# Kernel optimization log

Measured on AMD Instinct MI355X. Metric: run time of the kernel, lower is better.

Reference implementation:

```python
import jax, jax.numpy as jnp
import numpy as np
import math

B, T, D = 2, 2048, 1024
H, NL, DF = 16, 6, 4096
HD = D // H
EPS = 1e-5

def layer_norm(x, w, b):
    mu = jnp.mean(x, axis=-1, keepdims=True)
    var = jnp.mean((x - mu) ** 2, axis=-1, keepdims=True)
    return (x - mu) * jax.lax.rsqrt(var + EPS) * w + b

def setup_inputs() -> dict:
    key = jax.random.key(0)
    ks = jax.random.split(key, 12)
    def w(k, shape, scale=0.02):
        return jax.random.normal(k, shape, dtype=jnp.float32) * scale
    inp = {
        'sequences': jax.random.normal(ks[0], (B, T, D), dtype=jnp.float32),
        'Wq': w(ks[1], (NL, D, D)), 'bq': jnp.zeros((NL, D), jnp.float32),
        'Wk': w(ks[2], (NL, D, D)), 'bk': jnp.zeros((NL, D), jnp.float32),
        'Wv': w(ks[3], (NL, D, D)), 'bv': jnp.zeros((NL, D), jnp.float32),
        'Wo': w(ks[4], (NL, D, D)), 'bo': jnp.zeros((NL, D), jnp.float32),
        'Wz': w(ks[5], (NL, D, D)), 'bz': jnp.zeros((NL, D), jnp.float32),
        'Wr': w(ks[6], (NL, D, D)), 'br': jnp.zeros((NL, D), jnp.float32),
        'W1': w(ks[7], (NL, D, DF)), 'b1': jnp.zeros((NL, DF), jnp.float32),
        'W2': w(ks[8], (NL, DF, D)), 'b2': jnp.zeros((NL, D), jnp.float32),
        'ln1_w': jnp.ones((NL, D), jnp.float32), 'ln1_b': jnp.zeros((NL, D), jnp.float32),
        'ln2_w': jnp.ones((NL, D), jnp.float32), 'ln2_b': jnp.zeros((NL, D), jnp.float32),
        'lnf_w': jnp.ones((D,), jnp.float32), 'lnf_b': jnp.zeros((D,), jnp.float32),
    }
    return inp

def reference(sequences, Wq, bq, Wk, bk, Wv, bv, Wo, bo, Wz, bz, Wr, br,
              W1, b1, W2, b2, ln1_w, ln1_b, ln2_w, ln2_b, lnf_w, lnf_b):
    scale = 1.0 / math.sqrt(HD)
    causal = jnp.tril(jnp.ones((T, T), dtype=bool))  # mask[L:L+T, :L+T] with L=0
    x = sequences
    src = x
    for i in range(NL):
        xn = layer_norm(x, ln1_w[i], ln1_b[i])
        # QKV -> [B, H, T, HD]
        q = (xn @ Wq[i] + bq[i]).reshape(B, T, H, HD).transpose(0, 2, 1, 3)
        k = (xn @ Wk[i] + bk[i]).reshape(B, T, H, HD).transpose(0, 2, 1, 3)
        v = (xn @ Wv[i] + bv[i]).reshape(B, T, H, HD).transpose(0, 2, 1, 3)
        att = jnp.einsum('bhqd,bhkd->bhqk', q, k) * scale
        att = jnp.where(causal, att, -jnp.inf)
        att = jax.nn.softmax(att, axis=-1)
        y = jnp.einsum('bhqk,bhkd->bhqd', att, v)
        y = y.transpose(0, 2, 1, 3).reshape(B, T, D)
        x_attn = y @ Wo[i] + bo[i]
        z = jax.nn.sigmoid(xn @ Wz[i] + bz[i])
        r = jax.nn.sigmoid(xn @ Wr[i] + br[i])
        h_tilde = jnp.tanh(r * x_attn)
        x = (1.0 - z) * x + z * h_tilde
        xm = layer_norm(x, ln2_w[i], ln2_b[i])
        mlp = jax.nn.gelu(xm @ W1[i] + b1[i], approximate=False) @ W2[i] + b2[i]
        x = (1.0 - z) * x + z * mlp
        x = x + src
    x = layer_norm(x, lnf_w, lnf_b)
    return x
```

## Files before the change

### kernel.cpp

```cpp
#include <hip/hip_runtime.h>
#include <hip/hip_bf16.h>
#include <math.h>

#define B_ 2
#define T_ 2048
#define D_ 1024
#define H_ 16
#define NL_ 6
#define DF_ 4096
#define HD_ 64
#define M_ (B_*T_)

typedef __bf16 bf16;
typedef __attribute__((ext_vector_type(8))) __bf16 bf16x8;
typedef __attribute__((ext_vector_type(4))) float f32x4;
typedef __attribute__((ext_vector_type(16))) float f32x16;
typedef __attribute__((ext_vector_type(4))) unsigned u32x4;

#define BAR() __builtin_amdgcn_s_barrier()
#define LGKM0() asm volatile("s_waitcnt lgkmcnt(0)" ::: "memory")
#define VMC(n) asm volatile("s_waitcnt vmcnt(" #n ")" ::: "memory")

__device__ __forceinline__ void gload_lds16(const void* g, void* l) {
    __builtin_amdgcn_global_load_lds((const __attribute__((address_space(1))) void*)g,
                                     (__attribute__((address_space(3))) void*)l, 16, 0, 0);
}

__device__ __forceinline__ unsigned pk2(float a, float b) {
    bf16 lo = (bf16)a, hb = (bf16)b;
    return (unsigned)__builtin_bit_cast(unsigned short, lo) |
           ((unsigned)__builtin_bit_cast(unsigned short, hb) << 16);
}

__device__ __forceinline__ float4 ld4bf(const bf16* p) {
    float4 o;
    o.x = (float)p[0]; o.y = (float)p[1]; o.z = (float)p[2]; o.w = (float)p[3];
    return o;
}

template<bool OUT_BF16>
__global__ __launch_bounds__(256) void ln_kernel(const float* __restrict__ x,
        const float* __restrict__ w, const float* __restrict__ b,
        void* __restrict__ out) {
    const int row = blockIdx.x;
    const int t = threadIdx.x;
    const float4 xv = *(const float4*)(x + (long)row * D_ + t * 4);
    float s  = xv.x + xv.y + xv.z + xv.w;
    float sq = xv.x*xv.x + xv.y*xv.y + xv.z*xv.z + xv.w*xv.w;
    #pragma unroll
    for (int m = 32; m; m >>= 1) { s += __shfl_xor(s, m); sq += __shfl_xor(sq, m); }
    __shared__ float red[8];
    const int wid = t >> 6, lid = t & 63;
    if (lid == 0) { red[wid] = s; red[wid + 4] = sq; }
    __syncthreads();
    s  = red[0] + red[1] + red[2] + red[3];
    sq = red[4] + red[5] + red[6] + red[7];
    const float mu   = s * (1.0f / D_);
    const float var  = sq * (1.0f / D_) - mu * mu;
    const float rstd = rsqrtf(var + 1e-5f);
    const float4 wv = *(const float4*)(w + t * 4);
    const float4 bv = *(const float4*)(b + t * 4);
    float o0 = (xv.x - mu) * rstd * wv.x + bv.x;
    float o1 = (xv.y - mu) * rstd * wv.y + bv.y;
    float o2 = (xv.z - mu) * rstd * wv.z + bv.z;
    float o3 = (xv.w - mu) * rstd * wv.w + bv.w;
    if (OUT_BF16) {
        bf16* o = (bf16*)out + (long)row * D_ + t * 4;
        o[0] = (bf16)o0; o[1] = (bf16)o1; o[2] = (bf16)o2; o[3] = (bf16)o3;
    } else {
        float* o = (float*)out + (long)row * D_ + t * 4;
        o[0] = o0; o[1] = o1; o[2] = o2; o[3] = o3;
    }
}

__global__ __launch_bounds__(256) void wconv_all(
        const float* __restrict__ Wq, const float* __restrict__ Wk,
        const float* __restrict__ Wv, const float* __restrict__ Wz,
        const float* __restrict__ Wr, const float* __restrict__ Wo,
        const float* __restrict__ W1, const float* __restrict__ W2,
        bf16* __restrict__ wt) {
    __shared__ float s[32][33];
    const int bid = blockIdx.x;
    const float* src; bf16* dst; int t, K, nlg;
    if (bid < 6144) {
        const int m = bid >> 10; t = bid & 1023; K = 1024; nlg = 5;
        switch (m) {
            case 0: src = Wq; dst = wt; break;
            case 1: src = Wk; dst = wt + (1u << 20); break;
            case 2: src = Wv; dst = wt + (2u << 20); break;
            case 3: src = Wz; dst = wt + (3u << 20); break;
            case 4: src = Wr; dst = wt + (4u << 20); break;
            default: src = Wo; dst = wt + (5u << 20); break;
        }
    } else if (bid < 10240) {
        t = bid - 6144; K = 1024; nlg = 7; src = W1; dst = wt + (6u << 20);
    } else {
        t = bid - 10240; K = 4096; nlg = 5; src = W2; dst = wt + (10u << 20);
    }
    const int N = 1 << (nlg + 5);
    const int k0 = (t >> nlg) * 32, n0 = (t & ((1 << nlg) - 1)) * 32;
    const int c = threadIdx.x & 31, r8 = threadIdx.x >> 5;
    #pragma unroll
    for (int it = 0; it < 4; it++)
        s[r8 + it*8][c] = src[(long)(k0 + r8 + it*8) * N + n0 + c];
    __syncthreads();
    #pragma unroll
    for (int it = 0; it < 4; it++)
        dst[(long)(n0 + r8 + it*8) * K + k0 + c] = (bf16)s[c][r8 + it*8];
}

#define MFMA16(a, b, c) __builtin_amdgcn_mfma_f32_16x16x32_bf16(a, b, c, 0, 0, 0)
#define MFMA32(a, b, c) __builtin_amdgcn_mfma_f32_32x32x16_bf16(a, b, c, 0, 0, 0)

__device__ __forceinline__ void gemm128_core(const bf16* __restrict__ A, const bf16* __restrict__ Bt,
        const int Ks, const int NT, const int m0, const int n0, char* lds, f32x4 (&acc)[4][4]) {
    const int tid = threadIdx.x;
    const int lane = tid & 63, w = tid >> 6;
    const int wm = w >> 1, wn = w & 1;
    const int cl = lane & 15, gl = lane >> 4;
    const int srow = lane >> 2;
    const int sxc = (((lane & 3) ^ ((lane >> 3) & 3)) << 3);
    const bf16* pa0 = A  + (size_t)(m0 + w * 32 + srow) * Ks + sxc;
    const bf16* pa1 = pa0 + (size_t)16 * Ks;
    const bf16* pb  = Bt + (size_t)(n0 + w * 16 + srow) * Ks + sxc;
    char* laA = lds + w * 2048;
    char* laB = lds + 32768 + w * 1024;

#define STG(KT, BUF) do { \
    gload_lds16(pa0 + (size_t)(KT) * 32, laA + (BUF) * 16384); \
    gload_lds16(pa1 + (size_t)(KT) * 32, laA + (BUF) * 16384 + 1024); \
    gload_lds16(pb  + (size_t)(KT) * 32, laB + (BUF) * 8192); } while (0)

    STG(0, 0); STG(1, 1);
    VMC(3);

    const int xo  = ((gl ^ ((cl >> 1) & 3)) << 4);
    const int rdA = (wm * 64 + cl) * 64 + xo;
    const int rdB = (wn * 64 + cl) * 64 + xo;

    for (int kt = 0; kt < NT; ++kt) {
        const int buf = kt & 1;
        const char* sA = lds + buf * 16384;
        const char* sB = lds + 32768 + buf * 8192;
        BAR();
        bf16x8 a[4], b[4];
        #pragma unroll
        for (int mi = 0; mi < 4; mi++) a[mi] = *(const bf16x8*)(sA + rdA + mi * 1024);
        #pragma unroll
        for (int ni = 0; ni < 4; ni++) b[ni] = *(const bf16x8*)(sB + rdB + ni * 1024);
        LGKM0();
        BAR();
        if (kt + 2 < NT) STG(kt + 2, buf);
        __builtin_amdgcn_s_setprio(1);
        #pragma unroll
        for (int mi = 0; mi < 4; mi++)
            #pragma unroll
            for (int ni = 0; ni < 4; ni++)
                acc[mi][ni] = MFMA16(a[mi], b[ni], acc[mi][ni]);
        __builtin_amdgcn_s_setprio(0);
        if (kt + 2 < NT)      { VMC(3); }
        else if (kt + 1 < NT) { VMC(0); }
    }
#undef STG
}

__device__ __forceinline__ void gemm256_core(const bf16* __restrict__ A, const bf16* __restrict__ Bt,
        const int Ks, const int NT, const int m0, const int n0, char* lds, f32x4 (&acc)[8][4]) {
    const int tid = threadIdx.x;
    const int lane = tid & 63, w = tid >> 6;
    const int wm = w >> 2, wn = w & 3;
    const int cl = lane & 15, gl = lane >> 4;
    const int srow = lane >> 3;
    const int scol = ((lane & 7) ^ srow) * 8;
    const bf16* pa0 = A  + (size_t)(m0 + w * 16 + srow) * Ks + scol;
    const bf16* pa1 = pa0 + (size_t)8 * Ks;
    const bf16* pb0 = Bt + (size_t)(n0 + w * 16 + srow) * Ks + scol;
    const bf16* pb1 = pb0 + (size_t)8 * Ks;
    char* la = lds + w * 2048;
    char* lb = lds + 65536 + w * 2048;
    const size_t hA = (size_t)128 * Ks;

#define STGA(H, KT, BUF) do { \
    gload_lds16(pa0 + (size_t)(H) * hA + (size_t)(KT) * 64, la + (BUF) * 32768 + (H) * 16384); \
    gload_lds16(pa1 + (size_t)(H) * hA + (size_t)(KT) * 64, la + (BUF) * 32768 + (H) * 16384 + 1024); } while (0)
#define STGB(H, KT, BUF) do { \
    gload_lds16(pb0 + (size_t)(H) * hA + (size_t)(KT) * 64, lb + (BUF) * 32768 + (H) * 16384); \
    gload_lds16(pb1 + (size_t)(H) * hA + (size_t)(KT) * 64, lb + (BUF) * 32768 + (H) * 16384 + 1024); } while (0)

    STGA(0, 0, 0); STGA(1, 0, 0); STGB(0, 0, 0); STGB(1, 0, 0);
    STGB(0, 1, 1); STGA(0, 1, 1); STGA(1, 1, 1);
    VMC(6);
    BAR();

    const int X0  = (gl * 16) ^ ((cl & 7) << 4);
    const int rdA = (wm * 128 + cl) * 128 + X0;
    const int rdB = (wn * 64  + cl) * 128 + X0;

    for (int kt = 0; kt < NT; ++kt) {
        const int buf = kt & 1;
        const char* sAb = lds + buf * 32768;
        const char* sBb = lds + 65536 + buf * 32768;
        const bool st1 = (kt + 1 < NT), st2 = (kt + 2 < NT);
        bf16x8 a0[4][2], a4[4][2], b01[2][2], b23[2][2];
        #pragma unroll
        for (int mi = 0; mi < 4; mi++) {
            a0[mi][0] = *(const bf16x8*)(sAb + rdA + mi * 2048);
            a0[mi][1] = *(const bf16x8*)(sAb + (rdA ^ 64) + mi * 2048);
        }
        #pragma unroll
        for (int ni = 0; ni < 2; ni++) {
            b01[ni][0] = *(const bf16x8*)(sBb + rdB + ni * 2048);
            b01[ni][1] = *(const bf16x8*)(sBb + (rdB ^ 64) + ni * 2048);
        }
        if (st1) STGB(1, kt + 1, buf ^ 1);
        BAR(); LGKM0();
        __builtin_amdgcn_s_setprio(1);
        #pragma unroll
        for (int mi = 0; mi < 4; mi++)
            #pragma unroll
            for (int ni = 0; ni < 2; ni++) {
                acc[mi][ni] = MFMA16(a0[mi][0], b01[ni][0], acc[mi][ni]);
                acc[mi][ni] = MFMA16(a0[mi][1], b01[ni][1], acc[mi][ni]);
            }
        __builtin_amdgcn_s_setprio(0);
        BAR();
        #pragma unroll
        for (int mi = 0; mi < 4; mi++) {
            a4[mi][0] = *(const bf16x8*)(sAb + rdA + (mi + 4) * 2048);
            a4[mi][1] = *(const bf16x8*)(sAb + (rdA ^ 64) + (mi + 4) * 2048);
        }
        BAR(); LGKM0();
        __builtin_amdgcn_s_setprio(1);
        #pragma unroll
        for (int mi = 0; mi < 4; mi++)
            #pragma unroll
            for (int ni = 0; ni < 2; ni++) {
                acc[mi + 4][ni] = MFMA16(a4[mi][0], b01[ni][0], acc[mi + 4][ni]);
                acc[mi + 4][ni] = MFMA16(a4[mi][1], b01[ni][1], acc[mi + 4][ni]);
            }
        __builtin_amdgcn_s_setprio(0);
        BAR();
        #pragma unroll
        for (int ni = 0; ni < 2; ni++) {
            b23[ni][0] = *(const bf16x8*)(sBb + rdB + (ni + 2) * 2048);
            b23[ni][1] = *(const bf16x8*)(sBb + (rdB ^ 64) + (ni + 2) * 2048);
        }
        if (st2) STGA(0, kt + 2, buf);
        BAR(); LGKM0();
        __builtin_amdgcn_s_setprio(1);
        #pragma unroll
        for (int mi = 0; mi < 4; mi++)
            #pragma unroll
            for (int ni = 0; ni < 2; ni++) {
                acc[mi + 4][ni + 2] = MFMA16(a4[mi][0], b23[ni][0], acc[mi + 4][ni + 2]);
                acc[mi + 4][ni + 2] = MFMA16(a4[mi][1], b23[ni][1], acc[mi + 4][ni + 2]);
            }
        __builtin_amdgcn_s_setprio(0);
        BAR();
        if (st2) { STGA(1, kt + 2, buf); STGB(0, kt + 2, buf); }
        __builtin_amdgcn_s_setprio(1);
        #pragma unroll
        for (int mi = 0; mi < 4; mi++)
            #pragma unroll
            for (int ni = 0; ni < 2; ni++) {
                acc[mi][ni + 2] = MFMA16(a0[mi][0], b23[ni][0], acc[mi][ni + 2]);
                acc[mi][ni + 2] = MFMA16(a0[mi][1], b23[ni][1], acc[mi][ni + 2]);
            }
        __builtin_amdgcn_s_setprio(0);
        if (st2)      { VMC(6); }
        else if (st1) { VMC(0); }
        BAR();
    }
#undef STGA
#undef STGB
}

__global__ __launch_bounds__(512, 4) void gemm5_k(const bf16* __restrict__ A, const bf16* __restrict__ Bt,
        const float* __restrict__ bq, const float* __restrict__ bk, const float* __restrict__ bvv,
        const float* __restrict__ bz, const float* __restrict__ br,
        bf16* __restrict__ oq, bf16* __restrict__ ok, bf16* __restrict__ ov,
        bf16* __restrict__ oz, bf16* __restrict__ orr) {
    __shared__ __align__(16) char lds[49152];
    int bid = blockIdx.x;
    bid = (bid & 7) * 80 + (bid >> 3);
    const int m0 = (bid / 40) * 256, n0 = (bid % 40) * 128;
    f32x4 acc[4][4];
    #pragma unroll
    for (int i = 0; i < 4; i++)
        #pragma unroll
        for (int j = 0; j < 4; j++) acc[i][j] = (f32x4){0.f, 0.f, 0.f, 0.f};
    gemm128_core(A, Bt, 1024, 32, m0, n0, lds, acc);
    const int tid = threadIdx.x, lane = tid & 63, w = tid >> 6;
    const int wm = w >> 1, wn = w & 1, cl = lane & 15, gl = lane >> 4;
    const int seg = n0 >> 10;
    const int lc0 = (n0 & 1023) + wn * 64;
    const float* bias; int mode; bf16* outp;
    switch (seg) {
        case 0:  bias = bq;  mode = 0; outp = oq;  break;
        case 1:  bias = bk;  mode = 0; outp = ok;  break;
        case 2:  bias = bvv; mode = 1; outp = ov;  break;
        case 3:  bias = bz;  mode = 2; outp = oz;  break;
        default: bias = br;  mode = 2; outp = orr; break;
    }
    const float scl = (seg == 0) ? 0.125f : 1.0f;
    #pragma unroll
    for (int mi = 0; mi < 4; mi++) {
        #pragma unroll
        for (int ni = 0; ni < 4; ni++) {
            const int lcol = lc0 + ni * 16 + cl;
            const float bv = bias[lcol];
            #pragma unroll
            for (int r = 0; r < 4; r++) {
                const int row = m0 + wm * 64 + mi * 16 + gl * 4 + r;
                const float v = (acc[mi][ni][r] + bv) * scl;
                if (mode == 0) {
                    outp[(long)row * 1024 + lcol] = (bf16)v;
                } else if (mode == 1) {
                    outp[((long)(row >> 11) * 1024 + lcol) * T_ + (row & 2047)] = (bf16)v;
                } else {
                    outp[(long)row * 1024 + lcol] = (bf16)(1.0f / (1.0f + __expf(-v)));
                }
            }
        }
    }
}

__global__ __launch_bounds__(512, 2) void gemmG8_k(const bf16* __restrict__ A, const bf16* __restrict__ Bt,
        const float* __restrict__ bias, bf16* __restrict__ out) {
    __shared__ __align__(16) char lds[131072];
    int bid = blockIdx.x;
    bid = (bid & 7) * 32 + (bid >> 3);
    const int m0 = (bid >> 4) * 256, n0 = (bid & 15) * 256;
    f32x4 acc[8][4];
    #pragma unroll
    for (int i = 0; i < 8; i++)
        #pragma unroll
        for (int j = 0; j < 4; j++) acc[i][j] = (f32x4){0.f, 0.f, 0.f, 0.f};
    gemm256_core(A, Bt, 1024, 16, m0, n0, lds, acc);
    const int tid = threadIdx.x, lane = tid & 63, w = tid >> 6;
    const int wm = w >> 2, wn = w & 3, cl = lane & 15, gl = lane >> 4;
    #pragma unroll
    for (int mi = 0; mi < 8; mi++) {
        #pragma unroll
        for (int ni = 0; ni < 4; ni++) {
            const int col = n0 + wn * 64 + ni * 16 + cl;
            const float bv = bias[col];
            #pragma unroll
            for (int r = 0; r < 4; r++) {
                const int row = m0 + wm * 128 + mi * 16 + gl * 4 + r;
                float v = acc[mi][ni][r] + bv;
                v = 0.5f * v * (1.0f + erff(v * 0.70710678118f));
                out[(long)row * DF_ + col] = (bf16)v;
            }
        }
    }
}

__global__ __launch_bounds__(512, 2) void gemmP8_k(const bf16* __restrict__ A, const bf16* __restrict__ Bt,
        bf16* __restrict__ p0, bf16* __restrict__ p1, bf16* __restrict__ p2, bf16* __restrict__ p3) {
    __shared__ __align__(16) char lds[131072];
    int bid = blockIdx.x;
    bid = (bid & 7) * 32 + (bid >> 3);
    const int mt = bid >> 4, rest = bid & 15;
    const int nt = rest >> 2, s = rest & 3;
    const int m0 = mt * 256, n0 = nt * 256;
    f32x4 acc[8][4];
    #pragma unroll
    for (int i = 0; i < 8; i++)
        #pragma unroll
        for (int j = 0; j < 4; j++) acc[i][j] = (f32x4){0.f, 0.f, 0.f, 0.f};
    gemm256_core(A + s * 1024, Bt + s * 1024, 4096, 16, m0, n0, lds, acc);
    bf16* outp = (s == 0) ? p0 : (s == 1) ? p1 : (s == 2) ? p2 : p3;
    const int tid = threadIdx.x, lane = tid & 63, w = tid >> 6;
    const int wm = w >> 2, wn = w & 3, cl = lane & 15, gl = lane >> 4;
    #pragma unroll
    for (int mi = 0; mi < 8; mi++) {
        #pragma unroll
        for (int ni = 0; ni < 4; ni++) {
            const int col = n0 + wn * 64 + ni * 16 + cl;
            #pragma unroll
            for (int r = 0; r < 4; r++) {
                const int row = m0 + wm * 128 + mi * 16 + gl * 4 + r;
                outp[(long)row * 1024 + col] = (bf16)acc[mi][ni][r];
            }
        }
    }
}

__global__ __launch_bounds__(512, 4) void gemmWoG_kernel(const bf16* __restrict__ A,
        const bf16* __restrict__ Bt, const float* __restrict__ bias,
        float* __restrict__ x, const bf16* __restrict__ z, const bf16* __restrict__ rr) {
    __shared__ __align__(16) char lds[49152];
    int bid = blockIdx.x;
    bid = (bid & 7) * 16 + (bid >> 3);
    const int m0 = (bid >> 3) * 256, n0 = (bid & 7) * 128;
    f32x4 acc[4][4];
    #pragma unroll
    for (int i = 0; i < 4; i++)
        #pragma unroll
        for (int j = 0; j < 4; j++) acc[i][j] = (f32x4){0.f, 0.f, 0.f, 0.f};
    gemm128_core(A, Bt, 1024, 32, m0, n0, lds, acc);
    const int tid = threadIdx.x, lane = tid & 63, w = tid >> 6;
    const int wm = w >> 1, wn = w & 1, cl = lane & 15, gl = lane >> 4;
    #pragma unroll
    for (int mi = 0; mi < 4; mi++) {
        #pragma unroll
        for (int ni = 0; ni < 4; ni++) {
            const int col = n0 + wn * 64 + ni * 16 + cl;
            const float bv = bias[col];
            #pragma unroll
            for (int r = 0; r < 4; r++) {
                const int row = m0 + wm * 64 + mi * 16 + gl * 4 + r;
                const long idx = (long)row * D_ + col;
                const float xa = acc[mi][ni][r] + bv;
                const float zv = (float)z[idx];
                const float ht = tanhf((float)rr[idx] * xa);
                x[idx] = (1.f - zv) * x[idx] + zv * ht;
            }
        }
    }
}

__global__ __launch_bounds__(256, 2) void attn_kernel(const bf16* __restrict__ q,
        const bf16* __restrict__ k, const bf16* __restrict__ vT,
        bf16* __restrict__ y) {
    __shared__ __align__(16) char lds[32768];
    const int tid = threadIdx.x, wid = tid >> 6, lane = tid & 63;
    const int col = lane & 31, hi = lane >> 5;
    const int bid = blockIdx.x;
    const int xcd = bid & 7, idx = bid >> 3;
    const int bh = xcd + 8 * (idx & 3);
    const int sg = idx >> 2;
    const int g = (sg & 1) ? (sg >> 1) : (15 - (sg >> 1));
    const int qt = 4 * g + wid;
    const int qb = qt * 32;
    const int b = bh >> 4, h = bh & 15;
    const int NP = 2 * g + 2;
    const int nt64 = (qt >> 1) + 1;

    const bf16* qB = q  + (size_t)b * T_ * D_ + h * HD_;
    const bf16* kB = k  + (size_t)b * T_ * D_ + h * HD_;
    const bf16* vB = vT + (size_t)b * D_ * T_ + (size_t)h * HD_ * T_;

    const int sr = wid * 8 + (lane >> 3);
    const int sc = lane & 7;
    const bf16* kS0 = kB + (size_t)sr * D_ + 8 * (sc ^ (sr & 7));
    const bf16* kS1 = kS0 + (size_t)32 * D_;
    const bf16* vS0 = vB + (size_t)sr * T_ + 8 * (sc ^ (sr & 7));
    const bf16* vS1 = vS0 + (size_t)32 * T_;
    char* dK = lds + wid * 1024;
    char* dV = lds + 16384 + wid * 1024;

#define ASTG(J, BUF) do { \
    const size_t ko_ = (size_t)(J) * 64 * D_; \
    const size_t vo_ = (size_t)(J) * 64; \
    gload_lds16(kS0 + ko_, dK + (BUF) * 8192); \
    gload_lds16(kS1 + ko_, dK + (BUF) * 8192 + 4096); \
    gload_lds16(vS0 + vo_, dV + (BUF) * 8192); \
    gload_lds16(vS1 + vo_, dV + (BUF) * 8192 + 4096); } while (0)

    bf16x8 qf0, qf1, qf2, qf3;
    {
        const bf16* qp = qB + (size_t)(qb + col) * D_ + 8 * hi;
        qf0 = *(const bf16x8*)(qp);
        qf1 = *(const bf16x8*)(qp + 16);
        qf2 = *(const bf16x8*)(qp + 32);
        qf3 = *(const bf16x8*)(qp + 48);
    }

    f32x16 Od0, Od1;
    #pragma unroll
    for (int i = 0; i < 16; i++) { Od0[i] = 0.f; Od1[i] = 0.f; }
    float mrun = -INFINITY, lrun = 0.f;

    ASTG(0, 0);
    ASTG(1, 1);
    VMC(4);
    BAR();

    const int swz = col & 7;
    for (int j = 0; j < NP; ++j) {
        const int buf = j & 1;
        if (j < nt64) {
            const char* bK = lds + buf * 8192;
            const char* bV = lds + 16384 + buf * 8192;
            bf16x8 kf0[4], kf1[4], vf0[4], vf1[4];
            #pragma unroll
            for (int cs = 0; cs < 4; cs++) {
                const int ch = ((hi + 2 * cs) ^ swz) * 16;
                kf0[cs] = *(const bf16x8*)(bK + col * 128 + ch);
                kf1[cs] = *(const bf16x8*)(bK + (col + 32) * 128 + ch);
                vf0[cs] = *(const bf16x8*)(bV + col * 128 + ch);
                vf1[cs] = *(const bf16x8*)(bV + (col + 32) * 128 + ch);
            }
            f32x16 S0, S1;
            #pragma unroll
            for (int i = 0; i < 16; i++) { S0[i] = 0.f; S1[i] = 0.f; }
            S0 = MFMA32(kf0[0], qf0, S0); S0 = MFMA32(kf0[1], qf1, S0);
            S0 = MFMA32(kf0[2], qf2, S0); S0 = MFMA32(kf0[3], qf3, S0);
            S1 = MFMA32(kf1[0], qf0, S1); S1 = MFMA32(kf1[1], qf1, S1);
            S1 = MFMA32(kf1[2], qf2, S1); S1 = MFMA32(kf1[3], qf3, S1);
            float p[32];
            #pragma unroll
            for (int r = 0; r < 16; r++) { p[r] = S0[r]; p[16 + r] = S1[r]; }
            if (j == nt64 - 1) {
                const int qr = qb + col;
                #pragma unroll
                for (int r = 0; r < 32; r++) {
                    const int kvl = 64 * j + 32 * (r >> 4)
                                  + (r & 3) + 8 * ((r & 15) >> 2) + 4 * hi;
                    if (kvl > qr) p[r] = -3.0e38f;
                }
            }
            float tm = p[0];
            #pragma unroll
            for (int r = 1; r < 32; r++) tm = fmaxf(tm, p[r]);
            tm = fmaxf(tm, __shfl_xor(tm, 32));
            if (!__all(tm <= mrun + 8.f)) {
                const float mn = fmaxf(mrun, tm);
                const float al = __expf(mrun - mn);
                lrun *= al;
                #pragma unroll
                for (int i = 0; i < 16; i++) { Od0[i] *= al; Od1[i] *= al; }
                mrun = mn;
            }
            float ts = 0.f;
            #pragma unroll
            for (int r = 0; r < 32; r++) { p[r] = __expf(p[r] - mrun); ts += p[r]; }
            ts += __shfl_xor(ts, 32);
            lrun += ts;
            bf16x8 pbf[4];
            #pragma unroll
            for (int t = 0; t < 2; t++) {
                const unsigned pw0 = pk2(p[16*t+0],  p[16*t+1]),  pw1 = pk2(p[16*t+2],  p[16*t+3]);
                const unsigned pw2 = pk2(p[16*t+4],  p[16*t+5]),  pw3 = pk2(p[16*t+6],  p[16*t+7]);
                const unsigned pw4 = pk2(p[16*t+8],  p[16*t+9]),  pw5 = pk2(p[16*t+10], p[16*t+11]);
                const unsigned pw6 = pk2(p[16*t+12], p[16*t+13]), pw7 = pk2(p[16*t+14], p[16*t+15]);
                const unsigned px0 = __shfl_xor((int)pw0, 32), px1 = __shfl_xor((int)pw1, 32);
                const unsigned px2 = __shfl_xor((int)pw2, 32), px3 = __shfl_xor((int)pw3, 32);
                const unsigned px4 = __shfl_xor((int)pw4, 32), px5 = __shfl_xor((int)pw5, 32);
                const unsigned px6 = __shfl_xor((int)pw6, 32), px7 = __shfl_xor((int)pw7, 32);
                const u32x4 c0 = hi ? (u32x4){px2, px3, pw2, pw3} : (u32x4){pw0, pw1, px0, px1};
                const u32x4 c1 = hi ? (u32x4){px6, px7, pw6, pw7} : (u32x4){pw4, pw5, px4, px5};
                pbf[2*t]   = __builtin_bit_cast(bf16x8, c0);
                pbf[2*t+1] = __builtin_bit_cast(bf16x8, c1);
            }
            #pragma unroll
            for (int f = 0; f < 4; f++) {
                Od0 = MFMA32(vf0[f], pbf[f], Od0);
                Od1 = MFMA32(vf1[f], pbf[f], Od1);
            }
        }
        BAR();
        if (j + 2 < NP) { ASTG(j + 2, buf); VMC(4); }
        else            { VMC(0); }
        BAR();
    }

    const float inv = 1.0f / lrun;
    bf16* yr = y + (size_t)(b * T_ + qb + col) * D_ + h * HD_;
    #pragma unroll
    for (int rg = 0; rg < 4; rg++) {
        const int d0 = 8 * rg + 4 * hi;
        uint2 s0 = { pk2(Od0[4*rg] * inv, Od0[4*rg+1] * inv), pk2(Od0[4*rg+2] * inv, Od0[4*rg+3] * inv) };
        *(uint2*)(yr + d0) = s0;
        uint2 s1 = { pk2(Od1[4*rg] * inv, Od1[4*rg+1] * inv), pk2(Od1[4*rg+2] * inv, Od1[4*rg+3] * inv) };
        *(uint2*)(yr + 32 + d0) = s1;
    }
#undef ASTG
}

template<bool LN>
__global__ __launch_bounds__(256) void gate2ln_kernel(float* __restrict__ x,
        const bf16* __restrict__ z,
        const bf16* __restrict__ p0, const bf16* __restrict__ p1,
        const bf16* __restrict__ p2, const bf16* __restrict__ p3,
        const float* __restrict__ src, const float* __restrict__ b2,
        const float* __restrict__ lw, const float* __restrict__ lb,
        bf16* __restrict__ xn) {
    const int row = blockIdx.x, t = threadIdx.x;
    const long i = (long)row * D_ + t * 4;
    float4 xv = *(const float4*)(x + i);
    const float4 zv = ld4bf(z + i);
    const float4 a0 = ld4bf(p0 + i);
    const float4 a1 = ld4bf(p1 + i);
    const float4 a2 = ld4bf(p2 + i);
    const float4 a3 = ld4bf(p3 + i);
    const float4 sv = *(const float4*)(src + i);
    const float4 bb = *(const float4*)(b2 + t * 4);
    xv.x = (1.f - zv.x) * xv.x + zv.x * (a0.x + a1.x + a2.x + a3.x + bb.x) + sv.x;
    xv.y = (1.f - zv.y) * xv.y + zv.y * (a0.y + a1.y + a2.y + a3.y + bb.y) + sv.y;
    xv.z = (1.f - zv.z) * xv.z + zv.z * (a0.z + a1.z + a2.z + a3.z + bb.z) + sv.z;
    xv.w = (1.f - zv.w) * xv.w + zv.w * (a0.w + a1.w + a2.w + a3.w + bb.w) + sv.w;
    *(float4*)(x + i) = xv;
    if (LN) {
        float s  = xv.x + xv.y + xv.z + xv.w;
        float sq = xv.x*xv.x + xv.y*xv.y + xv.z*xv.z + xv.w*xv.w;
        #pragma unroll
        for (int m = 32; m; m >>= 1) { s += __shfl_xor(s, m); sq += __shfl_xor(sq, m); }
        __shared__ float red[8];
        const int wid = t >> 6, lid = t & 63;
        if (lid == 0) { red[wid] = s; red[wid + 4] = sq; }
        __syncthreads();
        s  = red[0] + red[1] + red[2] + red[3];
        sq = red[4] + red[5] + red[6] + red[7];
        const float mu   = s * (1.0f / D_);
        const float var  = sq * (1.0f / D_) - mu * mu;
        const float rstd = rsqrtf(var + 1e-5f);
        const float4 wv = *(const float4*)(lw + t * 4);
        const float4 bv = *(const float4*)(lb + t * 4);
        bf16* o = xn + i;
        o[0] = (bf16)((xv.x - mu) * rstd * wv.x + bv.x);
        o[1] = (bf16)((xv.y - mu) * rstd * wv.y + bv.y);
        o[2] = (bf16)((xv.z - mu) * rstd * wv.z + bv.z);
        o[3] = (bf16)((xv.w - mu) * rstd * wv.w + bv.w);
    }
}

extern "C" void kernel_launch(void* const* d_in, const int* in_sizes, int n_in,
                              void* d_out, int out_size, void* d_ws, size_t ws_size,
                              hipStream_t stream) {
    const float* seq   = (const float*)d_in[0];
    const float* Wq    = (const float*)d_in[1];  const float* bq = (const float*)d_in[2];
    const float* Wk    = (const float*)d_in[3];  const float* bk = (const float*)d_in[4];
    const float* Wv    = (const float*)d_in[5];  const float* bv = (const float*)d_in[6];
    const float* Wo    = (const float*)d_in[7];  const float* bo = (const float*)d_in[8];
    const float* Wz    = (const float*)d_in[9];  const float* bz = (const float*)d_in[10];
    const float* Wr    = (const float*)d_in[11]; const float* br = (const float*)d_in[12];
    const float* W1    = (const float*)d_in[13]; const float* b1 = (const float*)d_in[14];
    const float* W2    = (const float*)d_in[15]; const float* b2 = (const float*)d_in[16];
    const float* ln1w  = (const float*)d_in[17]; const float* ln1b = (const float*)d_in[18];
    const float* ln2w  = (const float*)d_in[19]; const float* ln2b = (const float*)d_in[20];
    const float* lnfw  = (const float*)d_in[21]; const float* lnfb = (const float*)d_in[22];

    char* ws = (char*)d_ws;
    float* x   = (float*)(ws);
    bf16*  z   = (bf16*)(ws + ((size_t)16 << 20));
    bf16*  r   = (bf16*)(ws + ((size_t)32 << 20));
    bf16*  xa  = (bf16*)(ws + ((size_t)48 << 20));
    bf16*  xn  = (bf16*)(ws + ((size_t)64 << 20));
    bf16*  qb_ = (bf16*)(ws + ((size_t)72 << 20));
    bf16*  kb_ = (bf16*)(ws + ((size_t)80 << 20));
    bf16*  vtb = (bf16*)(ws + ((size_t)88 << 20));
    bf16*  yb  = (bf16*)(ws + ((size_t)96 << 20));
    bf16*  h1  = (bf16*)(ws + ((size_t)104 << 20));
    bf16*  wt  = (bf16*)(ws + ((size_t)136 << 20));
    bf16*  pt2 = (bf16*)(ws + ((size_t)172 << 20));
    bf16*  pt3 = (bf16*)(ws + ((size_t)188 << 20));

    bf16* wto = wt + (5u << 20);
    bf16* wt1 = wt + (6u << 20);
    bf16* wt2 = wt + (10u << 20);

    hipMemcpyAsync(x, seq, (size_t)M_ * D_ * 4, hipMemcpyDeviceToDevice, stream);

    for (int i = 0; i < NL_; i++) {
        const long dd = (long)i * D_ * D_;
        wconv_all<<<14336, 256, 0, stream>>>(Wq + dd, Wk + dd, Wv + dd, Wz + dd,
                                             Wr + dd, Wo + dd,
                                             W1 + (long)i * D_ * DF_,
                                             W2 + (long)i * DF_ * D_, wt);
        if (i == 0)
            ln_kernel<true><<<M_, 256, 0, stream>>>(x, ln1w, ln1b, xn);
        gemm5_k<<<640, 512, 0, stream>>>(xn, wt,
                bq + i * D_, bk + i * D_, bv + i * D_, bz + i * D_, br + i * D_,
                qb_, kb_, vtb, z, r);
        attn_kernel<<<512, 256, 0, stream>>>(qb_, kb_, vtb, yb);
        gemmWoG_kernel<<<128, 512, 0, stream>>>(yb, wto, bo + i * D_, x, z, r);
        ln_kernel<true><<<M_, 256, 0, stream>>>(x, ln2w + i * D_, ln2b + i * D_, xn);
        gemmG8_k<<<256, 512, 0, stream>>>(xn, wt1, b1 + i * DF_, h1);
        gemmP8_k<<<256, 512, 0, stream>>>(h1, wt2, xa, r, pt2, pt3);
        if (i + 1 < NL_)
            gate2ln_kernel<true><<<M_, 256, 0, stream>>>(x, z, xa, r, pt2, pt3, seq, b2 + i * D_,
                    ln1w + (i + 1) * D_, ln1b + (i + 1) * D_, xn);
        else
            gate2ln_kernel<false><<<M_, 256, 0, stream>>>(x, z, xa, r, pt2, pt3, seq, b2 + i * D_,
                    nullptr, nullptr, nullptr);
    }
    ln_kernel<false><<<M_, 256, 0, stream>>>(x, lnfw, lnfb, d_out);
}
```

Measured before the change: 1.705 ms.

## Use 128x128 tiles with 256-thread blocks for output-projection gated GEMM

After: 1.671 ms. 2.0% less time.

```diff
diff --git a/kernel.cpp b/kernel.cpp
--- a/kernel.cpp
+++ b/kernel.cpp
@@ -164,6 +164,60 @@
 #undef STG
 }
 
+__device__ __forceinline__ void gemm64_core(const bf16* __restrict__ A, const bf16* __restrict__ Bt,
+        const int Ks, const int NT, const int m0, const int n0, char* lds, f32x4 (&acc)[4][4]) {
+    const int tid = threadIdx.x;
+    const int lane = tid & 63, w = tid >> 6;
+    const int wm = w >> 1, wn = w & 1;
+    const int cl = lane & 15, gl = lane >> 4;
+    const int srow = tid >> 2;
+    const int sxc = (((tid & 3) ^ ((tid >> 3) & 3)) << 3);
+    const bf16* pa0 = A  + (size_t)(m0 + srow) * Ks + sxc;
+    const bf16* pa1 = pa0 + (size_t)64 * Ks;
+    const bf16* pb0 = Bt + (size_t)(n0 + srow) * Ks + sxc;
+    const bf16* pb1 = pb0 + (size_t)64 * Ks;
+    char* laA = lds + w * 1024;
+    char* laB = lds + 16384 + w * 1024;
+
+#define STG(KT, BUF) do { \
+    gload_lds16(pa0 + (size_t)(KT) * 32, laA + (BUF) * 8192); \
+    gload_lds16(pa1 + (size_t)(KT) * 32, laA + (BUF) * 8192 + 4096); \
+    gload_lds16(pb0 + (size_t)(KT) * 32, laB + (BUF) * 8192); \
+    gload_lds16(pb1 + (size_t)(KT) * 32, laB + (BUF) * 8192 + 4096); } while (0)
+
+    STG(0, 0); STG(1, 1);
+    VMC(4);
+
+    const int xo  = ((gl ^ ((cl >> 1) & 3)) << 4);
+    const int rdA = (wm * 64 + cl) * 64 + xo;
+    const int rdB = (wn * 64 + cl) * 64 + xo;
+
+    for (int kt = 0; kt < NT; ++kt) {
+        const int buf = kt & 1;
+        const char* sA = lds + buf * 8192;
+        const char* sB = lds + 16384 + buf * 8192;
+        BAR();
+        bf16x8 a[4], b[4];
+        #pragma unroll
+        for (int mi = 0; mi < 4; mi++) a[mi] = *(const bf16x8*)(sA + rdA + mi * 1024);
+        #pragma unroll
+        for (int ni = 0; ni < 4; ni++) b[ni] = *(const bf16x8*)(sB + rdB + ni * 1024);
+        LGKM0();
+        BAR();
+        if (kt + 2 < NT) STG(kt + 2, buf);
+        __builtin_amdgcn_s_setprio(1);
+        #pragma unroll
+        for (int mi = 0; mi < 4; mi++)
+            #pragma unroll
+            for (int ni = 0; ni < 4; ni++)
+                acc[mi][ni] = MFMA16(a[mi], b[ni], acc[mi][ni]);
+        __builtin_amdgcn_s_setprio(0);
+        if (kt + 2 < NT)      { VMC(4); }
+        else if (kt + 1 < NT) { VMC(0); }
+    }
+#undef STG
+}
+
 __device__ __forceinline__ void gemm256_core(const bf16* __restrict__ A, const bf16* __restrict__ Bt,
         const int Ks, const int NT, const int m0, const int n0, char* lds, f32x4 (&acc)[8][4]) {
     const int tid = threadIdx.x;
@@ -387,19 +441,19 @@
     }
 }
 
-__global__ __launch_bounds__(512, 4) void gemmWoG_kernel(const bf16* __restrict__ A,
+__global__ __launch_bounds__(256, 4) void gemmWoG_kernel(const bf16* __restrict__ A,
         const bf16* __restrict__ Bt, const float* __restrict__ bias,
         float* __restrict__ x, const bf16* __restrict__ z, const bf16* __restrict__ rr) {
-    __shared__ __align__(16) char lds[49152];
+    __shared__ __align__(16) char lds[32768];
     int bid = blockIdx.x;
-    bid = (bid & 7) * 16 + (bid >> 3);
-    const int m0 = (bid >> 3) * 256, n0 = (bid & 7) * 128;
+    bid = (bid & 7) * 32 + (bid >> 3);
+    const int m0 = (bid >> 3) * 128, n0 = (bid & 7) * 128;
     f32x4 acc[4][4];
     #pragma unroll
     for (int i = 0; i < 4; i++)
         #pragma unroll
         for (int j = 0; j < 4; j++) acc[i][j] = (f32x4){0.f, 0.f, 0.f, 0.f};
-    gemm128_core(A, Bt, 1024, 32, m0, n0, lds, acc);
+    gemm64_core(A, Bt, 1024, 32, m0, n0, lds, acc);
     const int tid = threadIdx.x, lane = tid & 63, w = tid >> 6;
     const int wm = w >> 1, wn = w & 1, cl = lane & 15, gl = lane >> 4;
     #pragma unroll
@@ -666,7 +720,7 @@
                 bq + i * D_, bk + i * D_, bv + i * D_, bz + i * D_, br + i * D_,
                 qb_, kb_, vtb, z, r);
         attn_kernel<<<512, 256, 0, stream>>>(qb_, kb_, vtb, yb);
-        gemmWoG_kernel<<<128, 512, 0, stream>>>(yb, wto, bo + i * D_, x, z, r);
+        gemmWoG_kernel<<<256, 256, 0, stream>>>(yb, wto, bo + i * D_, x, z, r);
         ln_kernel<true><<<M_, 256, 0, stream>>>(x, ln2w + i * D_, ln2b + i * D_, xn);
         gemmG8_k<<<256, 512, 0, stream>>>(xn, wt1, b1 + i * DF_, h1);
         gemmP8_k<<<256, 512, 0, stream>>>(h1, wt2, xa, r, pt2, pt3);
```
